# Kernel optimization log

Hardware: AMD Instinct MI355X
Metric: run time of the kernel (lower is better)

## Reference

```python
import jax, jax.numpy as jnp
import numpy as np

B, T, D, H = 4, 4096, 128, 4
DH = D // H
FF = 2 * D
EPS = 1e-5


def _layernorm(x, g, b):
    mu = jnp.mean(x, axis=-1, keepdims=True)
    var = jnp.mean(jnp.square(x - mu), axis=-1, keepdims=True)
    return (x - mu) * jax.lax.rsqrt(var + EPS) * g + b


def setup_inputs() -> dict:
    key = jax.random.key(0)
    ks = jax.random.split(key, 12)

    def lin(k, fan_in, shape):
        return (jax.random.normal(k, shape, jnp.float32) / np.sqrt(fan_in)).astype(jnp.float32)

    return {
        "x": jax.random.normal(ks[0], (B, T, D), jnp.float32),
        "adj_mask": jax.random.randint(ks[1], (T, T), 0, 2).astype(bool),
        # weights stored (in, out); apply as x @ W + b
        "Wq": lin(ks[2], D, (D, D)), "bq": jnp.zeros((D,), jnp.float32),
        "Wk": lin(ks[3], D, (D, D)), "bk": jnp.zeros((D,), jnp.float32),
        "Wv": lin(ks[4], D, (D, D)), "bv": jnp.zeros((D,), jnp.float32),
        "Wo": lin(ks[5], D, (D, D)), "bo": jnp.zeros((D,), jnp.float32),
        "ln1_g": jnp.ones((D,), jnp.float32), "ln1_b": jnp.zeros((D,), jnp.float32),
        "W1": lin(ks[6], D, (D, FF)), "b1": jnp.zeros((FF,), jnp.float32),
        "W2": lin(ks[7], FF, (FF, D)), "b2": jnp.zeros((D,), jnp.float32),
        "ln2_g": jnp.ones((D,), jnp.float32), "ln2_b": jnp.zeros((D,), jnp.float32),
    }


def reference(x, adj_mask, Wq, bq, Wk, bk, Wv, bv, Wo, bo,
              ln1_g, ln1_b, W1, b1, W2, b2, ln2_g, ln2_b):
    b, t, d = x.shape
    q = (x @ Wq + bq).reshape(b, t, H, DH)
    k = (x @ Wk + bk).reshape(b, t, H, DH)
    v = (x @ Wv + bv).reshape(b, t, H, DH)

    # scores: (b, h, t, t)
    scores = jnp.einsum('bihd,bjhd->bhij', q, k) / np.sqrt(DH).astype(np.float32)
    full_mask = adj_mask | jnp.eye(t, dtype=bool)          # (t, t)
    scores = jnp.where(full_mask[None, None], scores, -jnp.inf)
    attn = jax.nn.softmax(scores, axis=-1)
    attn = jnp.where(jnp.isnan(attn), 0.0, attn)           # NaN cleanup as in source

    out = jnp.einsum('bhij,bjhd->bihd', attn, v).reshape(b, t, d)
    out = out @ Wo + bo
    x = _layernorm(x + out, ln1_g, ln1_b)
    ff = jax.nn.gelu(x @ W1 + b1, approximate=False) @ W2 + b2
    return _layernorm(x + ff, ln2_g, ln2_b)
```

## Files before the change

### kernel.cpp

```cpp
#include <hip/hip_runtime.h>
#include <hip/hip_bf16.h>
#include <math.h>


#define B_ 4
#define T_ 4096
#define D_ 128
#define H_ 4
#define DH_ 32
#define FF_ 256
#define M_ (B_*T_)

typedef unsigned short u16;
typedef __attribute__((ext_vector_type(8))) short bf16x8;
typedef __attribute__((ext_vector_type(4))) float f32x4;
typedef __attribute__((ext_vector_type(4))) u16 u16x4;

constexpr size_t OFF_FLAG  = 0;
constexpr size_t OFF_MASKW = 256;
constexpr size_t OFF_XB    = OFF_MASKW + 2097152;
constexpr size_t OFF_WQKVT = OFF_XB    + 4194304;
constexpr size_t OFF_WOT   = OFF_WQKVT + 98304;
constexpr size_t OFF_W1T   = OFF_WOT   + 32768;
constexpr size_t OFF_W2T   = OFF_W1T   + 65536;
constexpr size_t OFF_QW    = OFF_W2T   + 65536;
constexpr size_t OFF_KW    = OFF_QW    + 4194304;
constexpr size_t OFF_VT    = OFF_KW    + 4194304;
constexpr size_t OFF_AO    = OFF_VT    + 4194304;

__device__ __forceinline__ u16 f2bf(float f){
  unsigned u = __float_as_uint(f);
  u += 0x7FFFu + ((u >> 16) & 1u);
  return (u16)(u >> 16);
}

__device__ __forceinline__ float bf2f(u16 b){
  return __uint_as_float((unsigned)b << 16);
}

__device__ __forceinline__ bf16x8 load_frag(const u16* p){
  union { bf16x8 v; uint2 u[2]; } f;
  f.u[0] = *(const uint2*)(p);
  f.u[1] = *(const uint2*)(p + 16);
  return f.v;
}

__global__ void k_detect(const unsigned* m, int* flag, float* kmax2){
  if (threadIdx.x < 16) kmax2[threadIdx.x] = 0.f;
  __shared__ int s_i32, s_f32;
  if (threadIdx.x == 0){ s_i32 = 1; s_f32 = 1; }
  __syncthreads();
  int li = 1, lf = 1;
  for (int i = threadIdx.x; i < 16384; i += 256){
    unsigned w = m[i];
    li &= (w <= 1u);
    lf &= (w == 0u || w == 0x3F800000u);
  }
  if (!li) atomicAnd(&s_i32, 0);
  if (!lf) atomicAnd(&s_f32, 0);
  __syncthreads();
  if (threadIdx.x == 0) *flag = (s_i32 | s_f32);
}

__global__ void k_pack(const void* mask, const int* flag, unsigned* mw){
  int idx = blockIdx.x*256 + threadIdx.x;
  int i = idx >> 7, wj = idx & 127;
  unsigned w = 0;
  if (*flag){
    const unsigned* p = (const unsigned*)mask + (size_t)i*T_ + wj*32;
    #pragma unroll
    for (int c = 0; c < 32; c++) w |= (p[c] != 0u ? 1u : 0u) << c;
  } else {
    const unsigned char* p = (const unsigned char*)mask + (size_t)i*T_ + wj*32;
    #pragma unroll
    for (int c = 0; c < 32; c++) w |= (p[c] ? 1u : 0u) << c;
  }
  if ((i >> 5) == wj) w |= 1u << (i & 31);
  mw[idx] = w;
}

__global__ void k_conv_x(const float* x, u16* xb){
  int i = (blockIdx.x*256 + threadIdx.x)*4;
  float4 v = *(const float4*)(x + i);
  u16x4 o = { f2bf(v.x), f2bf(v.y), f2bf(v.z), f2bf(v.w) };
  *(u16x4*)(xb + i) = o;
}

__global__ void k_conv_w(const float* Wq, const float* Wk, const float* Wv, const float* Wo,
                         const float* W1, const float* W2,
                         u16* wqkvt, u16* wot, u16* w1t, u16* w2t){
  int idx = blockIdx.x*256 + threadIdx.x;
  if (idx < 49152){
    int n = idx >> 7, k = idx & 127;
    float v = (n < 128) ? Wq[k*128 + n] : (n < 256 ? Wk[k*128 + (n-128)] : Wv[k*128 + (n-256)]);
    wqkvt[idx] = f2bf(v);
  } else if (idx < 65536){
    int j = idx - 49152, n = j >> 7, k = j & 127;
    wot[j] = f2bf(Wo[k*128 + n]);
  } else if (idx < 98304){
    int j = idx - 65536, n = j >> 7, k = j & 127;
    w1t[j] = f2bf(W1[k*256 + n]);
  } else if (idx < 131072){
    int j = idx - 98304, n = j >> 8, k = j & 255;
    w2t[j] = f2bf(W2[k*128 + n]);
  }
}

__global__ __launch_bounds__(256) void k_qkv(const u16* xb, const u16* wt,
    const float* bq, const float* bk, const float* bv,
    u16* qw, u16* kw, u16* vt){
  __shared__ u16 st[16][392];
  const int wv = threadIdx.x >> 6, lane = threadIdx.x & 63;
  const int r15 = lane & 15, g = lane >> 4;
  const int m0 = blockIdx.x * 16;
  f32x4 acc[6] = {};
  const u16* ar = xb + (size_t)(m0 + r15)*D_ + 4*g;
  #pragma unroll
  for (int kk = 0; kk < D_; kk += 32){
    bf16x8 af = load_frag(ar + kk);
    #pragma unroll
    for (int nf = 0; nf < 6; nf++){
      const u16* br = wt + (size_t)(wv*96 + nf*16 + r15)*D_ + kk + 4*g;
      acc[nf] = __builtin_amdgcn_mfma_f32_16x16x32_bf16(af, load_frag(br), acc[nf], 0, 0, 0);
    }
  }
  #pragma unroll
  for (int nf = 0; nf < 6; nf++){
    int ncol = wv*96 + nf*16 + r15;
    float bias = (ncol < 128) ? bq[ncol] : (ncol < 256 ? bk[ncol-128] : bv[ncol-256]);
    float scl  = (ncol < 128) ? 0.17677669529663687f : 1.f;
    #pragma unroll
    for (int rr = 0; rr < 4; rr++)
      st[4*g + rr][ncol] = f2bf((acc[nf][rr] + bias) * scl);
  }
  __syncthreads();
  const int b = m0 >> 12, t0m = m0 & (T_-1);
  const int i = threadIdx.x;
  {
    const int t = i >> 4, c = i & 15, h = c >> 2, d0 = (c & 3)*8;
    uint4 v = *(const uint4*)&st[t][h*32 + d0];
    *(uint4*)(qw + ((size_t)(b*H_ + h)*T_ + (t0m + t))*DH_ + d0) = v;
  }
  {
    const int h = i >> 6, seg = (i >> 4) & 3, trow = i & 15;
    union { u16 e[8]; uint4 u; } v;
    #pragma unroll
    for (int sub = 0; sub < 8; sub++){
      int d = 16*(sub >> 2) + 4*seg + (sub & 3);
      v.e[sub] = st[trow][128 + h*32 + d];
    }
    *(uint4*)(kw + (size_t)(b*H_ + h)*T_*DH_ + (size_t)(t0m >> 4)*512 + seg*128 + trow*8) = v.u;
  }
  {
    const int bit4 = (t0m >> 4) & 1;
    #pragma unroll
    for (int cc = 0; cc < 2; cc++){
      const int c = i + cc*256;
      const int h = c >> 7, dlhi = (c >> 6) & 1, tq = (c >> 4) & 3, dl15 = c & 15;
      u16x4 v;
      #pragma unroll
      for (int j = 0; j < 4; j++)
        v[j] = st[tq*4 + j][256 + h*32 + dlhi*16 + dl15];
      *(u16x4*)(vt + (size_t)(b*H_ + h)*T_*DH_ + (size_t)(t0m >> 5)*1024
                + dlhi*512 + (size_t)(tq*16 + dl15)*8 + 4*bit4) = v;
    }
  }
}

__global__ void k_knorm(const u16* kw, float* kmax2){
  const int bh = blockIdx.x >> 4, slice = blockIdx.x & 15;
  const int t = slice*256 + threadIdx.x;
  const u16* base = kw + (size_t)bh*T_*DH_ + (size_t)(t >> 4)*512 + (t & 15)*8;
  float s = 0.f;
  #pragma unroll
  for (int g = 0; g < 4; g++){
    union { uint4 u4; u16 e[8]; } v;
    v.u4 = *(const uint4*)(base + g*128);
    #pragma unroll
    for (int j = 0; j < 8; j++){ float f = bf2f(v.e[j]); s += f*f; }
  }
  float mx = s;
  #pragma unroll
  for (int d = 1; d < 64; d <<= 1) mx = fmaxf(mx, __shfl_xor(mx, d));
  if ((threadIdx.x & 63) == 0) atomicMax((unsigned*)(kmax2 + bh), __float_as_uint(mx));
}

__global__ __launch_bounds__(256, 4) void k_attn14(const u16* qw, const u16* kw, const u16* vt,
    const unsigned* mw, const float* kmax2, u16* ao){
  const int wg = (blockIdx.x & 7)*128 + (blockIdx.x >> 3);
  const int wv = threadIdx.x >> 6, lane = threadIdx.x & 63;
  const int r15 = lane & 15, g = lane >> 4;
  const int bh = wg >> 6;
  const int q0 = (wg & 63)*64 + wv*16;
  const u16* qp = qw + (size_t)bh*T_*DH_;
  const u16* kl = kw + (size_t)bh*T_*DH_ + lane*8;
  const u16* vl = vt + (size_t)bh*T_*DH_ + lane*8;
  const unsigned* mrow = mw + (size_t)(q0 + r15)*(T_/32);
  const bf16x8 qf = load_frag(qp + (size_t)(q0 + r15)*DH_ + 4*g);
  float n0 = 0.f;
  #pragma unroll
  for (int j = 0; j < 8; j++){ float f = bf2f((u16)qf[j]); n0 += f*f; }
  n0 += __shfl_xor(n0, 16); n0 += __shfl_xor(n0, 32);
  const float bnd = sqrtf(n0 * kmax2[bh]) * 1.0001f + 1e-6f;
  union { u16 e[8]; bf16x8 v; } ones;
  #pragma unroll
  for (int j = 0; j < 8; j++) ones.e[j] = 0x3F80;
  f32x4 o0 = {}, o1 = {}, ol = {};
  for (int jb4 = 0; jb4 < T_; jb4 += 128){
    const uint4 wv4 = *(const uint4*)(mrow + (jb4 >> 5));
    #pragma unroll
    for (int ji = 0; ji < 4; ji++){
      const int jb = jb4 + ji*32;
      const unsigned w = ((const unsigned*)&wv4)[ji];
      const unsigned u = w >> (4*g);
      bf16x8 kf0 = *(const bf16x8*)(kl + (size_t)(jb >> 4)*512);
      bf16x8 kf1 = *(const bf16x8*)(kl + (size_t)((jb >> 4) + 1)*512);
      bf16x8 vf0 = *(const bf16x8*)(vl + (size_t)(jb >> 5)*1024);
      bf16x8 vf1 = *(const bf16x8*)(vl + (size_t)(jb >> 5)*1024 + 512);
      f32x4 c0, c1;
      #pragma unroll
      for (int rr = 0; rr < 4; rr++){
        c0[rr] = ((u >> rr) & 1u)        ? -bnd : -1e30f;
        c1[rr] = ((u >> (16 + rr)) & 1u) ? -bnd : -1e30f;
      }
      f32x4 s0 = __builtin_amdgcn_mfma_f32_16x16x32_bf16(kf0, qf, c0, 0, 0, 0);
      f32x4 s1 = __builtin_amdgcn_mfma_f32_16x16x32_bf16(kf1, qf, c1, 0, 0, 0);
      float p0[4], p1[4];
      #pragma unroll
      for (int rr = 0; rr < 4; rr++){
        p0[rr] = __expf(s0[rr]);
        p1[rr] = __expf(s1[rr]);
      }
      union { bf16x8 v; __hip_bfloat162 h2[4]; } pf;
      pf.h2[0] = __float22bfloat162_rn(make_float2(p0[0], p0[1]));
      pf.h2[1] = __float22bfloat162_rn(make_float2(p0[2], p0[3]));
      pf.h2[2] = __float22bfloat162_rn(make_float2(p1[0], p1[1]));
      pf.h2[3] = __float22bfloat162_rn(make_float2(p1[2], p1[3]));
      o0 = __builtin_amdgcn_mfma_f32_16x16x32_bf16(pf.v, vf0, o0, 0, 0, 0);
      o1 = __builtin_amdgcn_mfma_f32_16x16x32_bf16(pf.v, vf1, o1, 0, 0, 0);
      ol = __builtin_amdgcn_mfma_f32_16x16x32_bf16(pf.v, ones.v, ol, 0, 0, 0);
    }
  }
  const int b = bh >> 2, h = bh & 3;
  #pragma unroll
  for (int rr = 0; rr < 4; rr++){
    float li = ol[rr];
    float inv = li > 0.f ? 1.f/li : 0.f;
    size_t row = (size_t)(b*T_ + q0 + 4*g + rr)*D_;
    ao[row + h*DH_ + r15]      = f2bf(o0[rr]*inv);
    ao[row + h*DH_ + 16 + r15] = f2bf(o1[rr]*inv);
  }
}

__global__ __launch_bounds__(256) void k_tail(const u16* ao, const u16* wot, const float* bo,
    const float* x, const float* g1, const float* be1,
    const u16* w1t, const float* bf1, const u16* w2t, const float* b2,
    const float* g2, const float* be2, float* out){
  __shared__ float ly[16][132];
  __shared__ u16  lyb[16][136];
  __shared__ u16  lhb[16][264];
  __shared__ float rs[4][16], rq[4][16];
  const int wv = threadIdx.x >> 6, lane = threadIdx.x & 63;
  const int r15 = lane & 15, g = lane >> 4;
  const int m0 = blockIdx.x * 16;

  f32x4 accA[2] = {};
  const u16* ar = ao + (size_t)(m0 + r15)*D_ + 4*g;
  #pragma unroll
  for (int kk = 0; kk < D_; kk += 32){
    bf16x8 af = load_frag(ar + kk);
    #pragma unroll
    for (int nf = 0; nf < 2; nf++)
      accA[nf] = __builtin_amdgcn_mfma_f32_16x16x32_bf16(af,
          load_frag(wot + (size_t)((wv*2 + nf)*16 + r15)*D_ + kk + 4*g), accA[nf], 0, 0, 0);
  }
  float tA[2][4];
  #pragma unroll
  for (int rr = 0; rr < 4; rr++){
    float s1 = 0.f, s2 = 0.f;
    #pragma unroll
    for (int nf = 0; nf < 2; nf++){
      int col = (wv*2 + nf)*16 + r15;
      float t = accA[nf][rr] + bo[col] + x[(size_t)(m0 + 4*g + rr)*D_ + col];
      tA[nf][rr] = t; s1 += t; s2 += t*t;
    }
    #pragma unroll
    for (int d = 1; d < 16; d <<= 1){ s1 += __shfl_xor(s1, d); s2 += __shfl_xor(s2, d); }
    if (r15 == 0){ rs[wv][4*g + rr] = s1; rq[wv][4*g + rr] = s2; }
  }
  __syncthreads();
  #pragma unroll
  for (int rr = 0; rr < 4; rr++){
    int row = 4*g + rr;
    float S1 = rs[0][row] + rs[1][row] + rs[2][row] + rs[3][row];
    float S2 = rq[0][row] + rq[1][row] + rq[2][row] + rq[3][row];
    float mu = S1 * (1.f/D_);
    float var = fmaxf(S2 * (1.f/D_) - mu*mu, 0.f);
    float inv = rsqrtf(var + 1e-5f);
    #pragma unroll
    for (int nf = 0; nf < 2; nf++){
      int col = (wv*2 + nf)*16 + r15;
      float o = (tA[nf][rr] - mu)*inv*g1[col] + be1[col];
      ly[row][col] = o;
      lyb[row][col] = f2bf(o);
    }
  }
  __syncthreads();

  const int n0w = wv*64;
  f32x4 accB[4] = {};
  #pragma unroll
  for (int kk = 0; kk < D_; kk += 32){
    bf16x8 af = load_frag(&lyb[r15][kk + 4*g]);
    #pragma unroll
    for (int nf = 0; nf < 4; nf++)
      accB[nf] = __builtin_amdgcn_mfma_f32_16x16x32_bf16(af,
          load_frag(w1t + (size_t)(n0w + nf*16 + r15)*D_ + kk + 4*g), accB[nf], 0, 0, 0);
  }
  #pragma unroll
  for (int nf = 0; nf < 4; nf++){
    int col = n0w + nf*16 + r15;
    float bias = bf1[col];
    #pragma unroll
    for (int rr = 0; rr < 4; rr++){
      float vv = accB[nf][rr] + bias;
      float z2 = fminf(1.5957691216057308f*vv + 0.07135581778225507f*vv*vv*vv, 80.f);
      float t = __expf(z2);
      lhb[4*g + rr][col] = f2bf(vv * t / (t + 1.f));
    }
  }
  __syncthreads();

  f32x4 accC[2] = {};
  #pragma unroll
  for (int kk = 0; kk < FF_; kk += 32){
    bf16x8 af = load_frag(&lhb[r15][kk + 4*g]);
    #pragma unroll
    for (int nf = 0; nf < 2; nf++)
      accC[nf] = __builtin_amdgcn_mfma_f32_16x16x32_bf16(af,
          load_frag(w2t + (size_t)((wv*2 + nf)*16 + r15)*FF_ + kk + 4*g), accC[nf], 0, 0, 0);
  }
  float tC[2][4];
  #pragma unroll
  for (int rr = 0; rr < 4; rr++){
    float s1 = 0.f, s2 = 0.f;
    #pragma unroll
    for (int nf = 0; nf < 2; nf++){
      int col = (wv*2 + nf)*16 + r15;
      float t = accC[nf][rr] + b2[col] + ly[4*g + rr][col];
      tC[nf][rr] = t; s1 += t; s2 += t*t;
    }
    #pragma unroll
    for (int d = 1; d < 16; d <<= 1){ s1 += __shfl_xor(s1, d); s2 += __shfl_xor(s2, d); }
    if (r15 == 0){ rs[wv][4*g + rr] = s1; rq[wv][4*g + rr] = s2; }
  }
  __syncthreads();
  #pragma unroll
  for (int rr = 0; rr < 4; rr++){
    int row = 4*g + rr;
    float S1 = rs[0][row] + rs[1][row] + rs[2][row] + rs[3][row];
    float S2 = rq[0][row] + rq[1][row] + rq[2][row] + rq[3][row];
    float mu = S1 * (1.f/D_);
    float var = fmaxf(S2 * (1.f/D_) - mu*mu, 0.f);
    float inv = rsqrtf(var + 1e-5f);
    #pragma unroll
    for (int nf = 0; nf < 2; nf++){
      int col = (wv*2 + nf)*16 + r15;
      out[(size_t)(m0 + row)*D_ + col] = (tC[nf][rr] - mu)*inv*g2[col] + be2[col];
    }
  }
}

extern "C" void kernel_launch(void* const* d_in, const int* in_sizes, int n_in,
                              void* d_out, int out_size, void* d_ws, size_t ws_size,
                              hipStream_t stream){
  const float* x   = (const float*)d_in[0];
  const void*  msk = d_in[1];
  const float* Wq = (const float*)d_in[2];  const float* bq  = (const float*)d_in[3];
  const float* Wk = (const float*)d_in[4];  const float* bk  = (const float*)d_in[5];
  const float* Wv = (const float*)d_in[6];  const float* bv  = (const float*)d_in[7];
  const float* Wo = (const float*)d_in[8];  const float* bo  = (const float*)d_in[9];
  const float* g1 = (const float*)d_in[10]; const float* be1 = (const float*)d_in[11];
  const float* W1 = (const float*)d_in[12]; const float* bf1 = (const float*)d_in[13];
  const float* W2 = (const float*)d_in[14]; const float* b2  = (const float*)d_in[15];
  const float* g2 = (const float*)d_in[16]; const float* be2 = (const float*)d_in[17];

  char* ws = (char*)d_ws;
  int*      flag  = (int*)     (ws + OFF_FLAG);
  float*    kmax2 = (float*)   (ws + OFF_FLAG + 64);
  unsigned* mw    = (unsigned*)(ws + OFF_MASKW);
  u16* xb    = (u16*)(ws + OFF_XB);
  u16* wqkvt = (u16*)(ws + OFF_WQKVT);
  u16* wot   = (u16*)(ws + OFF_WOT);
  u16* w1t   = (u16*)(ws + OFF_W1T);
  u16* w2t   = (u16*)(ws + OFF_W2T);
  u16* qw    = (u16*)(ws + OFF_QW);
  u16* kw    = (u16*)(ws + OFF_KW);
  u16* vt    = (u16*)(ws + OFF_VT);
  u16* ao    = (u16*)(ws + OFF_AO);

  k_detect<<<1, 256, 0, stream>>>((const unsigned*)msk, flag, kmax2);
  k_pack  <<<(T_*T_/32)/256, 256, 0, stream>>>(msk, flag, mw);
  k_conv_x<<<(M_*D_/4)/256, 256, 0, stream>>>(x, xb);
  k_conv_w<<<131072/256, 256, 0, stream>>>(Wq, Wk, Wv, Wo, W1, W2, wqkvt, wot, w1t, w2t);
  k_qkv   <<<M_/16, 256, 0, stream>>>(xb, wqkvt, bq, bk, bv, qw, kw, vt);
  k_knorm <<<(B_*H_)*16, 256, 0, stream>>>(kw, kmax2);
  k_attn14<<<(B_*H_)*(T_/64), 256, 0, stream>>>(qw, kw, vt, mw, kmax2, ao);
  k_tail  <<<M_/16, 256, 0, stream>>>(ao, wot, bo, x, g1, be1, w1t, bf1, w2t, b2, g2, be2, (float*)d_out);
}
```

Measured before the change: 209.4 us.

## Fuse x conversion and key-norm into QKV, parallelise mask detect, vectorise packing

Converts x to bf16 inside the QKV kernel through shared memory, which removes the separate conversion kernel and its intermediate buffer. Computes per-head key-norm maxima from the staged tile inside the QKV kernel, dropping the separate knorm pass. Spreads mask-type detection over 64 blocks using wave votes and memsets for initialisation. Mask packing now uses vector loads and multiply tricks for bit extraction. Together these cut launch count and memory traffic in the preprocessing stages, at the cost of more atomics in QKV.

```diff
diff --git a/kernel.cpp b/kernel.cpp
--- a/kernel.cpp
+++ b/kernel.cpp
@@ -45,45 +45,39 @@
   return f.v;
 }
 
-__global__ void k_detect(const unsigned* m, int* flag, float* kmax2){
-  if (threadIdx.x < 16) kmax2[threadIdx.x] = 0.f;
-  __shared__ int s_i32, s_f32;
-  if (threadIdx.x == 0){ s_i32 = 1; s_f32 = 1; }
-  __syncthreads();
-  int li = 1, lf = 1;
-  for (int i = threadIdx.x; i < 16384; i += 256){
-    unsigned w = m[i];
-    li &= (w <= 1u);
-    lf &= (w == 0u || w == 0x3F800000u);
-  }
-  if (!li) atomicAnd(&s_i32, 0);
-  if (!lf) atomicAnd(&s_f32, 0);
-  __syncthreads();
-  if (threadIdx.x == 0) *flag = (s_i32 | s_f32);
-}
-
-__global__ void k_pack(const void* mask, const int* flag, unsigned* mw){
+__global__ void k_detect(const unsigned* m, unsigned* flags){
+  const int i = blockIdx.x*256 + threadIdx.x;
+  const unsigned w = m[i];
+  const int li = (w <= 1u);
+  const int lf = (w == 0u || w == 0x3F800000u);
+  if (!__all(li)){ if ((threadIdx.x & 63) == 0) atomicAnd(&flags[0], 0u); }
+  if (!__all(lf)){ if ((threadIdx.x & 63) == 0) atomicAnd(&flags[1], 0u); }
+}
+
+__global__ void k_pack(const void* mask, const unsigned* flags, unsigned* mw){
   int idx = blockIdx.x*256 + threadIdx.x;
   int i = idx >> 7, wj = idx & 127;
   unsigned w = 0;
-  if (*flag){
-    const unsigned* p = (const unsigned*)mask + (size_t)i*T_ + wj*32;
-    #pragma unroll
-    for (int c = 0; c < 32; c++) w |= (p[c] != 0u ? 1u : 0u) << c;
+  if (flags[0] | flags[1]){
+    const uint4* p = (const uint4*)((const unsigned*)mask + (size_t)i*T_ + wj*32);
+    #pragma unroll
+    for (int j = 0; j < 8; j++){
+      uint4 v = p[j];
+      w |= (unsigned)(v.x != 0u) << (4*j);
+      w |= (unsigned)(v.y != 0u) << (4*j + 1);
+      w |= (unsigned)(v.z != 0u) << (4*j + 2);
+      w |= (unsigned)(v.w != 0u) << (4*j + 3);
+    }
   } else {
-    const unsigned char* p = (const unsigned char*)mask + (size_t)i*T_ + wj*32;
-    #pragma unroll
-    for (int c = 0; c < 32; c++) w |= (p[c] ? 1u : 0u) << c;
+    const uint4* p = (const uint4*)((const unsigned char*)mask + (size_t)i*T_ + wj*32);
+    uint4 A = p[0], B = p[1];
+    #define NIB_(d) ((((d) & 0x01010101u) * 0x01020408u) >> 24)
+    w  =  NIB_(A.x)        | (NIB_(A.y) << 4)  | (NIB_(A.z) << 8)  | (NIB_(A.w) << 12)
+       | (NIB_(B.x) << 16) | (NIB_(B.y) << 20) | (NIB_(B.z) << 24) | (NIB_(B.w) << 28);
+    #undef NIB_
   }
   if ((i >> 5) == wj) w |= 1u << (i & 31);
   mw[idx] = w;
-}
-
-__global__ void k_conv_x(const float* x, u16* xb){
-  int i = (blockIdx.x*256 + threadIdx.x)*4;
-  float4 v = *(const float4*)(x + i);
-  u16x4 o = { f2bf(v.x), f2bf(v.y), f2bf(v.z), f2bf(v.w) };
-  *(u16x4*)(xb + i) = o;
 }
 
 __global__ void k_conv_w(const float* Wq, const float* Wk, const float* Wv, const float* Wo,
@@ -106,18 +100,29 @@
   }
 }
 
-__global__ __launch_bounds__(256) void k_qkv(const u16* xb, const u16* wt,
+__global__ __launch_bounds__(256) void k_qkv(const float* x, const u16* wt,
     const float* bq, const float* bk, const float* bv,
-    u16* qw, u16* kw, u16* vt){
+    u16* qw, u16* kw, u16* vt, float* kmax2){
+  __shared__ u16 xt[16][136];
   __shared__ u16 st[16][392];
   const int wv = threadIdx.x >> 6, lane = threadIdx.x & 63;
   const int r15 = lane & 15, g = lane >> 4;
   const int m0 = blockIdx.x * 16;
+  {
+    const int row = threadIdx.x >> 4, c0 = (threadIdx.x & 15) * 8;
+    const float* xp = x + (size_t)(m0 + row)*D_ + c0;
+    float4 a = *(const float4*)(xp);
+    float4 b = *(const float4*)(xp + 4);
+    u16x4 o1 = { f2bf(a.x), f2bf(a.y), f2bf(a.z), f2bf(a.w) };
+    u16x4 o2 = { f2bf(b.x), f2bf(b.y), f2bf(b.z), f2bf(b.w) };
+    *(u16x4*)&xt[row][c0]     = o1;
+    *(u16x4*)&xt[row][c0 + 4] = o2;
+  }
+  __syncthreads();
   f32x4 acc[6] = {};
-  const u16* ar = xb + (size_t)(m0 + r15)*D_ + 4*g;
   #pragma unroll
   for (int kk = 0; kk < D_; kk += 32){
-    bf16x8 af = load_frag(ar + kk);
+    bf16x8 af = load_frag(&xt[r15][kk + 4*g]);
     #pragma unroll
     for (int nf = 0; nf < 6; nf++){
       const u16* br = wt + (size_t)(wv*96 + nf*16 + r15)*D_ + kk + 4*g;
@@ -165,27 +170,16 @@
                 + dlhi*512 + (size_t)(tq*16 + dl15)*8 + 4*bit4) = v;
     }
   }
-}
-
-__global__ void k_knorm(const u16* kw, float* kmax2){
-  const int bh = blockIdx.x >> 4, slice = blockIdx.x & 15;
-  const int t = slice*256 + threadIdx.x;
-  const u16* base = kw + (size_t)bh*T_*DH_ + (size_t)(t >> 4)*512 + (t & 15)*8;
-  float s = 0.f;
-  #pragma unroll
-  for (int g = 0; g < 4; g++){
-    union { uint4 u4; u16 e[8]; } v;
-    v.u4 = *(const uint4*)(base + g*128);
-    #pragma unroll
-    for (int j = 0; j < 8; j++){ float f = bf2f(v.e[j]); s += f*f; }
-  }
-  float mx = s;
-  #pragma unroll
-  for (int d = 1; d < 64; d <<= 1) mx = fmaxf(mx, __shfl_xor(mx, d));
-  if ((threadIdx.x & 63) == 0) atomicMax((unsigned*)(kmax2 + bh), __float_as_uint(mx));
-}
-
-__global__ __launch_bounds__(256, 4) void k_attn14(const u16* qw, const u16* kw, const u16* vt,
+  if (i < 64){
+    const int t = i >> 2, h = i & 3;
+    float s = 0.f;
+    #pragma unroll
+    for (int d = 0; d < 32; d++){ float f = bf2f(st[t][128 + h*32 + d]); s += f*f; }
+    atomicMax((unsigned*)(kmax2 + (b*H_ + h)), __float_as_uint(s));
+  }
+}
+
+__global__ __launch_bounds__(256, 4) void k_attn15(const u16* qw, const u16* kw, const u16* vt,
     const unsigned* mw, const float* kmax2, u16* ao){
   const int wg = (blockIdx.x & 7)*128 + (blockIdx.x >> 3);
   const int wv = threadIdx.x >> 6, lane = threadIdx.x & 63;
@@ -386,10 +380,9 @@
   const float* g2 = (const float*)d_in[16]; const float* be2 = (const float*)d_in[17];
 
   char* ws = (char*)d_ws;
-  int*      flag  = (int*)     (ws + OFF_FLAG);
+  unsigned* flags = (unsigned*)(ws + OFF_FLAG);
   float*    kmax2 = (float*)   (ws + OFF_FLAG + 64);
   unsigned* mw    = (unsigned*)(ws + OFF_MASKW);
-  u16* xb    = (u16*)(ws + OFF_XB);
   u16* wqkvt = (u16*)(ws + OFF_WQKVT);
   u16* wot   = (u16*)(ws + OFF_WOT);
   u16* w1t   = (u16*)(ws + OFF_W1T);
@@ -399,12 +392,12 @@
   u16* vt    = (u16*)(ws + OFF_VT);
   u16* ao    = (u16*)(ws + OFF_AO);
 
-  k_detect<<<1, 256, 0, stream>>>((const unsigned*)msk, flag, kmax2);
-  k_pack  <<<(T_*T_/32)/256, 256, 0, stream>>>(msk, flag, mw);
-  k_conv_x<<<(M_*D_/4)/256, 256, 0, stream>>>(x, xb);
+  hipMemsetAsync(ws + OFF_FLAG, 1, 8, stream);
+  hipMemsetAsync(ws + OFF_FLAG + 64, 0, 64, stream);
+  k_detect<<<64, 256, 0, stream>>>((const unsigned*)msk, flags);
+  k_pack  <<<(T_*T_/32)/256, 256, 0, stream>>>(msk, flags, mw);
   k_conv_w<<<131072/256, 256, 0, stream>>>(Wq, Wk, Wv, Wo, W1, W2, wqkvt, wot, w1t, w2t);
-  k_qkv   <<<M_/16, 256, 0, stream>>>(xb, wqkvt, bq, bk, bv, qw, kw, vt);
-  k_knorm <<<(B_*H_)*16, 256, 0, stream>>>(kw, kmax2);
-  k_attn14<<<(B_*H_)*(T_/64), 256, 0, stream>>>(qw, kw, vt, mw, kmax2, ao);
+  k_qkv   <<<M_/16, 256, 0, stream>>>(x, wqkvt, bq, bk, bv, qw, kw, vt, kmax2);
+  k_attn15<<<(B_*H_)*(T_/64), 256, 0, stream>>>(qw, kw, vt, mw, kmax2, ao);
   k_tail  <<<M_/16, 256, 0, stream>>>(ao, wot, bo, x, g1, be1, w1t, bf1, w2t, b2, g2, be2, (float*)d_out);
 }
```

After: 361.2 us. 1.72x slower.
